# Optimization experiments

Hardware: AMD Instinct MI355X
Metric: run time of the kernel (lower is better)

Reference implementation:

```python
import jax, jax.numpy as jnp
import numpy as np

B, T, D = 4, 2048, 1024
H = 16
HD = D // H  # 64
SCALE = 1.0 / np.sqrt(HD).astype(np.float32)


def setup_inputs() -> dict:
    key = jax.random.key(0)
    ks = jax.random.split(key, 5)
    std = 0.02
    return {
        "x": jax.random.normal(ks[0], (B, T, D), dtype=jnp.float32),
        "wq": jax.random.normal(ks[1], (D, D), dtype=jnp.float32) * std,
        "wk": jax.random.normal(ks[2], (D, D), dtype=jnp.float32) * std,
        "wv": jax.random.normal(ks[3], (D, D), dtype=jnp.float32) * std,
        "wo": jax.random.normal(ks[4], (D, D), dtype=jnp.float32) * std,
    }


def _shape(t):
    # [B,T,D] -> [B,H,T,HD]
    Bt, Tt, _ = t.shape
    return t.reshape(Bt, Tt, H, HD).transpose(0, 2, 1, 3)


def reference(x, wq, wk, wv, wo):
    # Linear layers are y = x @ W^T (torch nn.Linear semantics, no bias)
    q = _shape(x @ wq.T)  # [B,H,T,HD]
    k = _shape(x @ wk.T)
    v = _shape(x @ wv.T)
    att = jnp.einsum("bhqd,bhkd->bhqk", q, k) * SCALE  # [B,H,T,T]
    # causal mask: -inf strictly above diagonal
    causal = jnp.triu(jnp.full((T, T), -jnp.inf, dtype=att.dtype), k=1)
    att = att + causal[None, None, :, :]
    att = jax.nn.softmax(att.astype(jnp.float32), axis=-1).astype(att.dtype)
    # dropout prob = 0.0 -> identity
    y = jnp.einsum("bhqk,bhkd->bhqd", att, v)  # [B,H,T,HD]
    y = y.transpose(0, 2, 1, 3).reshape(B, T, D)
    return y @ wo.T
```

## Files before the change

kernel.cpp:

```cpp
#include <hip/hip_runtime.h>
#include <hip/hip_bf16.h>

#define BB 4
#define TT 2048
#define DDIM 1024
#define HH 16
#define HD 64

typedef __bf16 bf16_t;
typedef __bf16 bf16x4 __attribute__((ext_vector_type(4)));
typedef __bf16 bf16x8 __attribute__((ext_vector_type(8)));
typedef float f32x4 __attribute__((ext_vector_type(4)));

#define GLOAD_LDS(gp, lp) \
    __builtin_amdgcn_global_load_lds( \
        (const __attribute__((address_space(1))) void*)(gp), \
        (__attribute__((address_space(3))) void*)(lp), 16, 0, 0)

__global__ __launch_bounds__(256) void cvt_f32_bf16(
    const float* __restrict__ src, bf16_t* __restrict__ dst, size_t n8)
{
    size_t i = (size_t)blockIdx.x * blockDim.x + threadIdx.x;
    const size_t stride = (size_t)gridDim.x * blockDim.x;
    for (; i < n8; i += stride) {
        const f32x4 a = ((const f32x4*)src)[2 * i];
        const f32x4 b = ((const f32x4*)src)[2 * i + 1];
        bf16x8 v;
#pragma unroll
        for (int j = 0; j < 4; j++) { v[j] = (bf16_t)a[j]; v[4 + j] = (bf16_t)b[j]; }
        ((bf16x8*)dst)[i] = v;
    }
}

__global__ __launch_bounds__(256) void cvt_wpack(
    const float* __restrict__ s0, const float* __restrict__ s1,
    const float* __restrict__ s2, const float* __restrict__ s3,
    bf16_t* __restrict__ dst)
{
    const size_t n8 = (size_t)4 * DDIM * DDIM / 8;
    size_t i = (size_t)blockIdx.x * blockDim.x + threadIdx.x;
    const size_t stride = (size_t)gridDim.x * blockDim.x;
    for (; i < n8; i += stride) {
        const int sel = (int)(i >> 17);
        const float* s = sel == 0 ? s0 : sel == 1 ? s1 : sel == 2 ? s2 : s3;
        const size_t off8 = i & ((1u << 17) - 1);
        const f32x4 a = ((const f32x4*)s)[2 * off8];
        const f32x4 b = ((const f32x4*)s)[2 * off8 + 1];
        bf16x8 v;
#pragma unroll
        for (int j = 0; j < 4; j++) { v[j] = (bf16_t)a[j]; v[4 + j] = (bf16_t)b[j]; }
        ((bf16x8*)dst)[i] = v;
    }
}

__device__ __forceinline__ void stage8(const bf16_t* __restrict__ g, int ld,
                                       bf16_t* __restrict__ ldsbase, int lane)
{
    const int rr = lane >> 3;
    const int cc = (lane & 7) ^ rr;
    GLOAD_LDS(&g[(size_t)rr * ld + cc * 8], ldsbase);
}

__global__ __launch_bounds__(256) void gemm_qkv(
    const bf16_t* __restrict__ A, const bf16_t* __restrict__ Wqkv,
    bf16_t* __restrict__ Qo, bf16_t* __restrict__ Ko, bf16_t* __restrict__ Vto,
    int M, int K)
{
    __shared__ alignas(16) bf16_t As[2][128 * 64];
    __shared__ alignas(16) bf16_t Bs[2][128 * 64];

    const int tid  = threadIdx.x;
    const int lane = tid & 63;
    const int w    = tid >> 6;
    const int quad = lane >> 4;
    const int l15  = lane & 15;
    const int wm   = (w >> 1) * 64;
    const int wn   = (w & 1) * 64;

    const int nwg = gridDim.x * gridDim.y;
    const int cpx = nwg >> 3;
    int id = blockIdx.y * gridDim.x + blockIdx.x;
    id = (id & 7) * cpx + (id >> 3);
    const int tileN = (id % 24) * 128;
    const int tileM = (id / 24) * 128;

    const f32x4 vzero = {0.f, 0.f, 0.f, 0.f};
    f32x4 acc[4][4];
#pragma unroll
    for (int i = 0; i < 4; i++)
#pragma unroll
        for (int j = 0; j < 4; j++) acc[i][j] = vzero;

    const int par8 = l15 & 7;

#pragma unroll
    for (int q = 0; q < 4; q++) {
        const int r0 = w * 32 + q * 8;
        stage8(&A[(size_t)(tileM + r0) * K], K, &As[0][r0 * 64], lane);
        stage8(&Wqkv[(size_t)(tileN + r0) * K], K, &Bs[0][r0 * 64], lane);
    }
    __syncthreads();

    const int NT = K >> 6;
    for (int t = 0; t < NT; ++t) {
        const int cur = t & 1;
        if (t + 1 < NT) {
            const int k0 = (t + 1) << 6;
#pragma unroll
            for (int q = 0; q < 4; q++) {
                const int r0 = w * 32 + q * 8;
                stage8(&A[(size_t)(tileM + r0) * K + k0], K,
                       &As[cur ^ 1][r0 * 64], lane);
                stage8(&Wqkv[(size_t)(tileN + r0) * K + k0], K,
                       &Bs[cur ^ 1][r0 * 64], lane);
            }
        }

#pragma unroll
        for (int ss = 0; ss < 2; ss++) {
            const int phys = ((ss * 4 + quad) ^ par8) << 3;
            bf16x8 af[4], bf[4];
#pragma unroll
            for (int i = 0; i < 4; i++)
                af[i] = *(bf16x8*)&As[cur][(wm + i * 16 + l15) * 64 + phys];
#pragma unroll
            for (int j = 0; j < 4; j++)
                bf[j] = *(bf16x8*)&Bs[cur][(wn + j * 16 + l15) * 64 + phys];
            __builtin_amdgcn_s_setprio(1);
#pragma unroll
            for (int i = 0; i < 4; i++)
#pragma unroll
                for (int j = 0; j < 4; j++)
                    acc[i][j] = __builtin_amdgcn_mfma_f32_16x16x32_bf16(
                        af[i], bf[j], acc[i][j], 0, 0, 0);
            __builtin_amdgcn_s_setprio(0);
        }
        __syncthreads();
    }

    const int region = tileN >> 10;
    const float osc = (region == 0) ? 0.125f * 1.44269504f : 1.0f;
#pragma unroll
    for (int i = 0; i < 4; i++) {
        const int row = tileM + wm + i * 16 + quad * 4;
#pragma unroll
        for (int j = 0; j < 4; j++) {
            const int ncol = tileN + wn + j * 16 + l15;
            if (region == 2) {
                const int cl = ncol - 2048;
                const int h = cl >> 6, d = cl & 63;
                const int bb = row >> 11, tloc = row & (TT - 1);
                bf16x4 pk;
#pragma unroll
                for (int r = 0; r < 4; r++) pk[r] = (bf16_t)acc[i][j][r];
                *(bf16x4*)&Vto[(((size_t)bb * HH + h) * HD + d) * TT + tloc] = pk;
            } else {
                bf16_t* dst = (region == 0) ? Qo : Ko;
                const int cl = ncol & 1023;
#pragma unroll
                for (int r = 0; r < 4; r++)
                    dst[(size_t)(row + r) * DDIM + cl] = (bf16_t)(acc[i][j][r] * osc);
            }
        }
    }
}

__global__ __launch_bounds__(256) void gemm_out(
    const bf16_t* __restrict__ A, const bf16_t* __restrict__ Bm,
    float* __restrict__ C, int M, int N, int K)
{
    __shared__ alignas(16) bf16_t As[2][128 * 64];
    __shared__ alignas(16) bf16_t Bs[2][128 * 64];

    const int tid  = threadIdx.x;
    const int lane = tid & 63;
    const int w    = tid >> 6;
    const int quad = lane >> 4;
    const int l15  = lane & 15;
    const int wm   = (w >> 1) * 64;
    const int wn   = (w & 1) * 64;

    const int nwg = gridDim.x * gridDim.y;
    const int cpx = nwg >> 3;
    int id = blockIdx.y * gridDim.x + blockIdx.x;
    id = (id & 7) * cpx + (id >> 3);
    const int tileN = (id % 8) * 128;
    const int tileM = (id / 8) * 128;

    const f32x4 vzero = {0.f, 0.f, 0.f, 0.f};
    f32x4 acc[4][4];
#pragma unroll
    for (int i = 0; i < 4; i++)
#pragma unroll
        for (int j = 0; j < 4; j++) acc[i][j] = vzero;

    const int par8 = l15 & 7;

#pragma unroll
    for (int q = 0; q < 4; q++) {
        const int r0 = w * 32 + q * 8;
        stage8(&A[(size_t)(tileM + r0) * K], K, &As[0][r0 * 64], lane);
        stage8(&Bm[(size_t)(tileN + r0) * K], K, &Bs[0][r0 * 64], lane);
    }
    __syncthreads();

    const int NT = K >> 6;
    for (int t = 0; t < NT; ++t) {
        const int cur = t & 1;
        if (t + 1 < NT) {
            const int k0 = (t + 1) << 6;
#pragma unroll
            for (int q = 0; q < 4; q++) {
                const int r0 = w * 32 + q * 8;
                stage8(&A[(size_t)(tileM + r0) * K + k0], K,
                       &As[cur ^ 1][r0 * 64], lane);
                stage8(&Bm[(size_t)(tileN + r0) * K + k0], K,
                       &Bs[cur ^ 1][r0 * 64], lane);
            }
        }

#pragma unroll
        for (int ss = 0; ss < 2; ss++) {
            const int phys = ((ss * 4 + quad) ^ par8) << 3;
            bf16x8 af[4], bf[4];
#pragma unroll
            for (int i = 0; i < 4; i++)
                af[i] = *(bf16x8*)&As[cur][(wm + i * 16 + l15) * 64 + phys];
#pragma unroll
            for (int j = 0; j < 4; j++)
                bf[j] = *(bf16x8*)&Bs[cur][(wn + j * 16 + l15) * 64 + phys];
            __builtin_amdgcn_s_setprio(1);
#pragma unroll
            for (int i = 0; i < 4; i++)
#pragma unroll
                for (int j = 0; j < 4; j++)
                    acc[i][j] = __builtin_amdgcn_mfma_f32_16x16x32_bf16(
                        af[i], bf[j], acc[i][j], 0, 0, 0);
            __builtin_amdgcn_s_setprio(0);
        }
        __syncthreads();
    }

#pragma unroll
    for (int i = 0; i < 4; i++) {
#pragma unroll
        for (int r = 0; r < 4; r++) {
            const int row = tileM + wm + i * 16 + quad * 4 + r;
#pragma unroll
            for (int j = 0; j < 4; j++)
                C[(size_t)row * N + tileN + wn + j * 16 + l15] = acc[i][j][r];
        }
    }
}

__global__ __launch_bounds__(256, 3) void attn_causal(
    const bf16_t* __restrict__ Q, const bf16_t* __restrict__ Kg,
    const bf16_t* __restrict__ Vt_g, bf16_t* __restrict__ Y)
{
    __shared__ alignas(16) bf16_t Ks[2 * 64 * 64];
    __shared__ alignas(16) bf16_t Vt[2 * 64 * 64];
    __shared__ alignas(16) bf16_t Ps[4][32 * 72];

    const int tid  = threadIdx.x;
    const int lane = tid & 63;
    const int w    = tid >> 6;
    const int quad = lane >> 4;
    const int l15  = lane & 15;
    const int bh   = blockIdx.x;
    const int sp   = blockIdx.y;
    const int b = bh >> 4, h = bh & 15;

    const int stg_row = tid >> 3;
    const int stg_c8  = (tid & 7) * 8;
    const int stg_off = stg_row * 64 + ((((tid & 7) ^ (stg_row & 7))) << 3);
    const int par8 = l15 & 7;

    const f32x4 vzero = {0.f, 0.f, 0.f, 0.f};
    bf16x8 ones;
#pragma unroll
    for (int j = 0; j < 8; j++) ones[j] = (l15 == 0) ? (bf16_t)1.0f : (bf16_t)0.0f;

    const bf16_t* kg0 = &Kg[(size_t)(b * TT + stg_row) * DDIM + h * 64 + stg_c8];
    const bf16_t* vg0 = &Vt_g[((size_t)bh * HD + stg_row) * TT + stg_c8];

#pragma unroll 1
    for (int half = 0; half < 2; half++) {
        const int strip = half ? (15 - sp) : sp;
        const int qbase = strip * 128;

        bf16x8 qf[2][2];
#pragma unroll
        for (int mi = 0; mi < 2; mi++) {
            const size_t rq =
                (size_t)(b * TT + qbase + w * 32 + mi * 16 + l15) * DDIM + h * 64;
            qf[mi][0] = *(const bf16x8*)&Q[rq + quad * 8];
            qf[mi][1] = *(const bf16x8*)&Q[rq + 32 + quad * 8];
        }

        f32x4 o[2][4], o4[2];
#pragma unroll
        for (int mi = 0; mi < 2; mi++) {
#pragma unroll
            for (int c = 0; c < 4; c++) o[mi][c] = vzero;
            o4[mi] = vzero;
        }

        const int nkt = 2 * strip + 2;

        bf16x8 kreg[2], vreg[2];
#pragma unroll
        for (int p = 0; p < 2; p++) {
            kreg[p] = *(const bf16x8*)&kg0[(size_t)(p * 32) * DDIM];
            vreg[p] = *(const bf16x8*)&vg0[(size_t)(p * 32) * TT];
        }

#pragma unroll 1
        for (int kt = 0; kt < nkt; kt++) {
            const int kbase = kt * 64;
            const int coff = (kt & 1) * (64 * 64);
#pragma unroll
            for (int p = 0; p < 2; p++) {
                *(bf16x8*)&Ks[coff + stg_off + p * 32 * 64] = kreg[p];
                *(bf16x8*)&Vt[coff + stg_off + p * 32 * 64] = vreg[p];
            }
            if (kt + 1 < nkt) {
                const int nb = (kt + 1) * 64;
#pragma unroll
                for (int p = 0; p < 2; p++) {
                    kreg[p] = *(const bf16x8*)&kg0[(size_t)(nb + p * 32) * DDIM];
                    vreg[p] = *(const bf16x8*)&vg0[(size_t)(p * 32) * TT + nb];
                }
            }
            __syncthreads();

            f32x4 s[2][4];
            __builtin_amdgcn_s_setprio(1);
#pragma unroll
            for (int c = 0; c < 4; c++) {
                const int krow = (c * 16 + l15) * 64;
                bf16x8 kf0 = *(bf16x8*)&Ks[coff + krow + ((quad ^ par8) << 3)];
                bf16x8 kf1 = *(bf16x8*)&Ks[coff + krow + (((4 + quad) ^ par8) << 3)];
#pragma unroll
                for (int mi = 0; mi < 2; mi++) {
                    f32x4 t = __builtin_amdgcn_mfma_f32_16x16x32_bf16(
                        qf[mi][0], kf0, vzero, 0, 0, 0);
                    s[mi][c] = __builtin_amdgcn_mfma_f32_16x16x32_bf16(
                        qf[mi][1], kf1, t, 0, 0, 0);
                }
            }
            __builtin_amdgcn_s_setprio(0);

#pragma unroll
            for (int mi = 0; mi < 2; mi++) {
                const int qlow = qbase + w * 32 + mi * 16;
                const bool need = (kbase + 63 > qlow);
#pragma unroll
                for (int r = 0; r < 4; r++) {
                    const int qrow = qlow + quad * 4 + r;
                    const int prow = mi * 16 + quad * 4 + r;
#pragma unroll
                    for (int c = 0; c < 4; c++) {
                        float sv = s[mi][c][r];
                        if (need && (kbase + c * 16 + l15 > qrow)) sv = -1e30f;
                        const int pchunk = (c * 2 + (l15 >> 3)) ^ (prow >> 2);
                        Ps[w][prow * 72 + (pchunk << 3) + (l15 & 7)] =
                            (bf16_t)__builtin_amdgcn_exp2f(sv);
                    }
                }
            }

            __builtin_amdgcn_s_setprio(1);
#pragma unroll
            for (int ss = 0; ss < 2; ss++) {
                bf16x8 pf[2];
#pragma unroll
                for (int mi = 0; mi < 2; mi++) {
                    const int m = mi * 16 + l15;
                    pf[mi] = *(bf16x8*)&Ps[w][m * 72 +
                                              ((((ss * 4 + quad) ^ (m >> 2)) & 7) << 3)];
                }
#pragma unroll
                for (int c = 0; c < 4; c++) {
                    bf16x8 vf = *(bf16x8*)&Vt[coff + (c * 16 + l15) * 64 +
                                              (((ss * 4 + quad) ^ par8) << 3)];
#pragma unroll
                    for (int mi = 0; mi < 2; mi++)
                        o[mi][c] = __builtin_amdgcn_mfma_f32_16x16x32_bf16(
                            pf[mi], vf, o[mi][c], 0, 0, 0);
                }
#pragma unroll
                for (int mi = 0; mi < 2; mi++)
                    o4[mi] = __builtin_amdgcn_mfma_f32_16x16x32_bf16(
                        pf[mi], ones, o4[mi], 0, 0, 0);
            }
            __builtin_amdgcn_s_setprio(0);
        }

#pragma unroll
        for (int mi = 0; mi < 2; mi++) {
#pragma unroll
            for (int r = 0; r < 4; r++) {
                const float lsum = __shfl(o4[mi][r], lane & 48, 64);
                const float inv = 1.0f / lsum;
                const int q = qbase + w * 32 + mi * 16 + quad * 4 + r;
#pragma unroll
                for (int c = 0; c < 4; c++)
                    Y[(size_t)(b * TT + q) * DDIM + h * 64 + c * 16 + l15] =
                        (bf16_t)(o[mi][c][r] * inv);
            }
        }
    }
}

extern "C" void kernel_launch(void* const* d_in, const int* in_sizes, int n_in,
                              void* d_out, int out_size, void* d_ws, size_t ws_size,
                              hipStream_t stream) {
    (void)in_sizes; (void)n_in; (void)out_size;
    const float* x  = (const float*)d_in[0];
    float* out = (float*)d_out;

    const int M = BB * TT;
    const size_t REGION = (size_t)M * DDIM;
    const size_t WREG   = (size_t)DDIM * DDIM;
    const size_t BATCH  = (size_t)TT * DDIM;
    bf16_t* ws = (bf16_t*)d_ws;

    if (ws_size >= (72ull << 20)) {
        bf16_t* xb  = ws;
        bf16_t* wpk = ws + REGION;
        bf16_t* Qb  = wpk + 4 * WREG;
        bf16_t* Kb  = Qb + REGION;
        bf16_t* Vtb = Kb + REGION;

        cvt_f32_bf16<<<1024, 256, 0, stream>>>(x, xb, REGION / 8);
        cvt_wpack<<<512, 256, 0, stream>>>(
            (const float*)d_in[1], (const float*)d_in[2],
            (const float*)d_in[3], (const float*)d_in[4], wpk);

        gemm_qkv<<<dim3(24, M / 128), 256, 0, stream>>>(
            xb, wpk, Qb, Kb, Vtb, M, DDIM);
        attn_causal<<<dim3(BB * HH, 8), 256, 0, stream>>>(Qb, Kb, Vtb, Qb);
        gemm_out<<<dim3(8, M / 128), 256, 0, stream>>>(
            Qb, wpk + 3 * WREG, out, M, DDIM, DDIM);
    } else {
        bf16_t* wpk = ws;
        bf16_t* xbb = ws + 4 * WREG;
        bf16_t* Qb  = xbb + BATCH;
        bf16_t* Kb  = Qb + BATCH;
        bf16_t* Vtb = Kb + BATCH;

        cvt_wpack<<<512, 256, 0, stream>>>(
            (const float*)d_in[1], (const float*)d_in[2],
            (const float*)d_in[3], (const float*)d_in[4], wpk);

        for (int b = 0; b < BB; b++) {
            const float* x_b = x + (size_t)b * BATCH;
            float* out_b = out + (size_t)b * BATCH;
            cvt_f32_bf16<<<512, 256, 0, stream>>>(x_b, xbb, BATCH / 8);
            gemm_qkv<<<dim3(24, TT / 128), 256, 0, stream>>>(
                xbb, wpk, Qb, Kb, Vtb, TT, DDIM);
            attn_causal<<<dim3(HH, 8), 256, 0, stream>>>(Qb, Kb, Vtb, Qb);
            gemm_out<<<dim3(8, TT / 128), 256, 0, stream>>>(
                Qb, wpk + 3 * WREG, out_b, TT, DDIM, DDIM);
        }
    }
}
```

Before: 244.8 us.

## Enlarge QKV GEMM tile to 256x128 with triple-buffered LDS pipeline

```diff
diff --git a/kernel.cpp b/kernel.cpp
--- a/kernel.cpp
+++ b/kernel.cpp
@@ -61,13 +61,13 @@
     GLOAD_LDS(&g[(size_t)rr * ld + cc * 8], ldsbase);
 }
 
-__global__ __launch_bounds__(256) void gemm_qkv(
+__global__ __launch_bounds__(512) void gemm_qkv(
     const bf16_t* __restrict__ A, const bf16_t* __restrict__ Wqkv,
     bf16_t* __restrict__ Qo, bf16_t* __restrict__ Ko, bf16_t* __restrict__ Vto,
     int M, int K)
 {
-    __shared__ alignas(16) bf16_t As[2][128 * 64];
-    __shared__ alignas(16) bf16_t Bs[2][128 * 64];
+    __shared__ alignas(16) bf16_t As[3][256 * 64];
+    __shared__ alignas(16) bf16_t Bs[3][128 * 64];
 
     const int tid  = threadIdx.x;
     const int lane = tid & 63;
@@ -82,7 +82,7 @@
     int id = blockIdx.y * gridDim.x + blockIdx.x;
     id = (id & 7) * cpx + (id >> 3);
     const int tileN = (id % 24) * 128;
-    const int tileM = (id / 24) * 128;
+    const int tileM = (id / 24) * 256;
 
     const f32x4 vzero = {0.f, 0.f, 0.f, 0.f};
     f32x4 acc[4][4];
@@ -93,28 +93,37 @@
 
     const int par8 = l15 & 7;
 
-#pragma unroll
-    for (int q = 0; q < 4; q++) {
-        const int r0 = w * 32 + q * 8;
-        stage8(&A[(size_t)(tileM + r0) * K], K, &As[0][r0 * 64], lane);
-        stage8(&Wqkv[(size_t)(tileN + r0) * K], K, &Bs[0][r0 * 64], lane);
-    }
-    __syncthreads();
+#define STAGE_QKV(t_, b_) do { \
+        const int k0_ = (t_) << 6; \
+        _Pragma("unroll") \
+        for (int q_ = 0; q_ < 4; q_++) { \
+            const int r0_ = w * 32 + q_ * 8; \
+            stage8(&A[(size_t)(tileM + r0_) * K + k0_], K, \
+                   &As[b_][r0_ * 64], lane); \
+        } \
+        _Pragma("unroll") \
+        for (int q_ = 0; q_ < 2; q_++) { \
+            const int r0_ = w * 16 + q_ * 8; \
+            stage8(&Wqkv[(size_t)(tileN + r0_) * K + k0_], K, \
+                   &Bs[b_][r0_ * 64], lane); \
+        } \
+    } while (0)
+
+    STAGE_QKV(0, 0);
+    STAGE_QKV(1, 1);
 
     const int NT = K >> 6;
+#pragma unroll 1
     for (int t = 0; t < NT; ++t) {
-        const int cur = t & 1;
-        if (t + 1 < NT) {
-            const int k0 = (t + 1) << 6;
-#pragma unroll
-            for (int q = 0; q < 4; q++) {
-                const int r0 = w * 32 + q * 8;
-                stage8(&A[(size_t)(tileM + r0) * K + k0], K,
-                       &As[cur ^ 1][r0 * 64], lane);
-                stage8(&Wqkv[(size_t)(tileN + r0) * K + k0], K,
-                       &Bs[cur ^ 1][r0 * 64], lane);
-            }
-        }
+        if (t + 1 < NT) asm volatile("s_waitcnt vmcnt(6)" ::: "memory");
+        else            asm volatile("s_waitcnt vmcnt(0)" ::: "memory");
+        __builtin_amdgcn_s_barrier();
+        if (t + 2 < NT) {
+            const int nb = (t + 2) % 3;
+            STAGE_QKV(t + 2, nb);
+        }
+        const bf16_t* as = &As[t % 3][0];
+        const bf16_t* bs = &Bs[t % 3][0];
 
 #pragma unroll
         for (int ss = 0; ss < 2; ss++) {
@@ -122,10 +131,10 @@
             bf16x8 af[4], bf[4];
 #pragma unroll
             for (int i = 0; i < 4; i++)
-                af[i] = *(bf16x8*)&As[cur][(wm + i * 16 + l15) * 64 + phys];
+                af[i] = *(bf16x8*)&as[(wm + i * 16 + l15) * 64 + phys];
 #pragma unroll
             for (int j = 0; j < 4; j++)
-                bf[j] = *(bf16x8*)&Bs[cur][(wn + j * 16 + l15) * 64 + phys];
+                bf[j] = *(bf16x8*)&bs[(wn + j * 16 + l15) * 64 + phys];
             __builtin_amdgcn_s_setprio(1);
 #pragma unroll
             for (int i = 0; i < 4; i++)
@@ -135,8 +144,8 @@
                         af[i], bf[j], acc[i][j], 0, 0, 0);
             __builtin_amdgcn_s_setprio(0);
         }
-        __syncthreads();
-    }
+    }
+#undef STAGE_QKV
 
     const int region = tileN >> 10;
     const float osc = (region == 0) ? 0.125f * 1.44269504f : 1.0f;
@@ -437,7 +446,7 @@
             (const float*)d_in[1], (const float*)d_in[2],
             (const float*)d_in[3], (const float*)d_in[4], wpk);
 
-        gemm_qkv<<<dim3(24, M / 128), 256, 0, stream>>>(
+        gemm_qkv<<<dim3(24, M / 256), 512, 0, stream>>>(
             xb, wpk, Qb, Kb, Vtb, M, DDIM);
         attn_causal<<<dim3(BB * HH, 8), 256, 0, stream>>>(Qb, Kb, Vtb, Qb);
         gemm_out<<<dim3(8, M / 128), 256, 0, stream>>>(
@@ -457,7 +466,7 @@
             const float* x_b = x + (size_t)b * BATCH;
             float* out_b = out + (size_t)b * BATCH;
             cvt_f32_bf16<<<512, 256, 0, stream>>>(x_b, xbb, BATCH / 8);
-            gemm_qkv<<<dim3(24, TT / 128), 256, 0, stream>>>(
+            gemm_qkv<<<dim3(24, TT / 256), 512, 0, stream>>>(
                 xbb, wpk, Qb, Kb, Vtb, TT, DDIM);
             attn_causal<<<dim3(HH, 8), 256, 0, stream>>>(Qb, Kb, Vtb, Qb);
             gemm_out<<<dim3(8, TT / 128), 256, 0, stream>>>(
```

Result: slower. 256.7 us (+4.9%).
